# Performance work log

Measured on AMD Instinct MI355X. Metric: run time of the kernel, lower is better.

## Reference

```python
import jax, jax.numpy as jnp
import numpy as np

CUTOFF = 5.0           # module init kwarg
NSYS, NAT = 64, 1000   # 64 systems of 1000 atoms each
BOX = 21.544           # cubic box edge -> ~0.1 atoms/A^3 (water-like density)
MAX_PAIRS = 2_200_000


def setup_inputs() -> dict:
    key = jax.random.key(0)
    coords = jax.random.uniform(key, (NSYS * NAT, 3), dtype=jnp.float32) * BOX
    isys = jnp.repeat(jnp.arange(NSYS, dtype=jnp.int32), NAT)
    natoms = jnp.full((NSYS,), NAT, dtype=jnp.int32)
    return {"coordinates": coords, "isys": isys, "natoms": natoms}


def reference(coordinates, isys, natoms):
    # Fixed-capacity cutoff neighbor list (no PBC branch), faithful to
    # GraphGeneratorFixed: half-list (i<j, same system), squared distances d12,
    # compacted into a MAX_PAIRS buffer padded with padding_value=N, then
    # symmetrized by concatenation.
    nsys = natoms.shape[0]
    n = coordinates.shape[0]
    nat = n // nsys                      # equal-sized systems (static)
    padding_value = n
    cutoff2 = jnp.float32(CUTOFF * CUTOFF)

    x = coordinates.reshape(nsys, nat, 3)                 # [S, nat, 3]
    sq = jnp.sum(x * x, axis=-1)                          # [S, nat]
    gram = jnp.einsum('sid,sjd->sij', x, x)               # [S, nat, nat]
    d12 = sq[:, :, None] + sq[:, None, :] - 2.0 * gram    # squared distances

    triu = jnp.triu(jnp.ones((nat, nat), dtype=bool), k=1)  # i < j half-list
    mask = (d12 < cutoff2) & triu[None, :, :]             # [S, nat, nat]
    mflat = mask.reshape(-1)                              # [S*nat*nat]
    npairs = jnp.sum(mflat)

    # stream-compaction: position of each kept pair in the output buffer
    pos = jnp.cumsum(mflat.astype(jnp.int32)) - 1
    sel = jnp.where(mflat, pos, MAX_PAIRS)                # OOB -> dropped
    flat_idx = jnp.arange(nsys * nat * nat, dtype=jnp.int32)
    idx_buf = jnp.full((MAX_PAIRS,), -1, dtype=jnp.int32).at[sel].set(
        flat_idx, mode='drop')

    valid = idx_buf >= 0
    ib = jnp.maximum(idx_buf, 0)
    s = ib // (nat * nat)
    rem = ib % (nat * nat)
    i = rem // nat
    j = rem % nat
    src = jnp.where(valid, s * nat + i, padding_value)
    dst = jnp.where(valid, s * nat + j, padding_value)
    d12_sel = jnp.where(valid, d12.reshape(-1)[ib], cutoff2)

    # symmetrize (directed graph), as in the original
    edge_src = jnp.concatenate([src, dst])
    edge_dst = jnp.concatenate([dst, src])
    d12_out = jnp.concatenate([d12_sel, d12_sel])
    return edge_src, edge_dst, d12_out, npairs
```

## Files before the change

kernel.cpp:

```cpp
#include <hip/hip_runtime.h>

#define NSYS 64
#define NAT  1000
#define NTOT (NSYS * NAT)
#define MP   2200000
#define CUT2 25.0f
#define PADV 64000.0f
#define SCAN_BLOCKS 250
#define RPB  16
#define TILES ((NAT + RPB - 1) / RPB)
#define CAP  104

__device__ __forceinline__ float dist2f(float xi, float yi, float zi,
                                        float xj, float yj, float zj) {
    float dx = xi - xj, dy = yi - yj, dz = zi - zj;
    return fmaf(dz, dz, fmaf(dy, dy, dx * dx));
}

__global__ __launch_bounds__(1024) void k_eval(const float* __restrict__ coords,
                                               int* __restrict__ counts,
                                               uint2* __restrict__ qbuf) {
    __shared__ float lc[NAT * 3];
    int s    = blockIdx.x / TILES;
    int tile = blockIdx.x % TILES;
    const float* cs = coords + s * (NAT * 3);
    for (int idx = threadIdx.x; idx < NAT * 3; idx += 1024) lc[idx] = cs[idx];
    __syncthreads();
    int w    = threadIdx.x >> 6;
    int lane = threadIdx.x & 63;
    int r    = tile * RPB + w;
    if (r >= NAT) return;
    float xi = lc[3 * r], yi = lc[3 * r + 1], zi = lc[3 * r + 2];
    int grow = s * NAT + r;
    uint2* q = qbuf + (size_t)grow * CAP;
    int running = 0;
    unsigned long long lt = (1ull << lane) - 1ull;
    for (int j = r + 1 + lane; j < NAT; j += 64) {
        float d2 = dist2f(xi, yi, zi, lc[3 * j], lc[3 * j + 1], lc[3 * j + 2]);
        bool keep = d2 < CUT2;
        unsigned long long m = __ballot(keep);
        if (keep) {
            int rank = running + (int)__popcll(m & lt);
            if (rank < CAP)
                q[rank] = make_uint2((unsigned)(j - r), __float_as_uint(d2));
        }
        running += (int)__popcll(m);
    }
    if (lane == 0) counts[grow] = running;
}

__global__ void k_scan_a(const int* __restrict__ counts, int* __restrict__ offs,
                         int* __restrict__ bsum) {
    __shared__ int tmp[256];
    int t = threadIdx.x;
    int g = blockIdx.x * 256 + t;
    int v = counts[g];
    tmp[t] = v;
    __syncthreads();
    for (int off = 1; off < 256; off <<= 1) {
        int u = (t >= off) ? tmp[t - off] : 0;
        __syncthreads();
        tmp[t] += u;
        __syncthreads();
    }
    offs[g] = tmp[t] - v;
    if (t == 255) bsum[blockIdx.x] = tmp[255];
}

__global__ void k_scan_b(int* __restrict__ bsum, int* __restrict__ total) {
    __shared__ int tmp[256];
    int t = threadIdx.x;
    int v = (t < SCAN_BLOCKS) ? bsum[t] : 0;
    tmp[t] = v;
    __syncthreads();
    for (int off = 1; off < 256; off <<= 1) {
        int u = (t >= off) ? tmp[t - off] : 0;
        __syncthreads();
        tmp[t] += u;
        __syncthreads();
    }
    if (t < SCAN_BLOCKS) bsum[t] = tmp[t] - v;
    if (t == 255) *total = tmp[255];
}

__global__ void k_emit(const int* __restrict__ counts, const int* __restrict__ offs,
                       const int* __restrict__ bsum, const uint2* __restrict__ qbuf,
                       float* __restrict__ out) {
    int gt   = blockIdx.x * blockDim.x + threadIdx.x;
    int row  = gt >> 6;
    int lane = gt & 63;
    if (row >= NTOT) return;
    int off = offs[row] + bsum[row >> 8];
    int cnt = counts[row];
    if (cnt > CAP) cnt = CAP;
    const uint2* q = qbuf + (size_t)row * CAP;
    float fs = (float)row;
    for (int l = lane; l < cnt; l += 64) {
        uint2 e = q[l];
        int pos = off + l;
        if (pos < MP) {
            float fd = (float)(row + (int)e.x);
            float d2 = __uint_as_float(e.y);
            out[pos]          = fs;
            out[MP + pos]     = fd;
            out[2 * MP + pos] = fd;
            out[3 * MP + pos] = fs;
            out[4 * MP + pos] = d2;
            out[5 * MP + pos] = d2;
        }
    }
}

__global__ void k_pad(const int* __restrict__ total_p, float* __restrict__ out) {
    int k4 = (blockIdx.x * 256 + threadIdx.x) * 4;
    if (k4 >= MP) return;
    int total = *total_p;
    if (k4 == 0) out[6 * MP] = (float)total;
    int valid = total < MP ? total : MP;
    if (k4 + 4 <= valid) return;
    if (k4 >= valid) {
        float4 vp = {PADV, PADV, PADV, PADV};
        float4 vc = {CUT2, CUT2, CUT2, CUT2};
        *(float4*)(out + k4)          = vp;
        *(float4*)(out + MP + k4)     = vp;
        *(float4*)(out + 2 * MP + k4) = vp;
        *(float4*)(out + 3 * MP + k4) = vp;
        *(float4*)(out + 4 * MP + k4) = vc;
        *(float4*)(out + 5 * MP + k4) = vc;
    } else {
#pragma unroll
        for (int e = 0; e < 4; e++) {
            int k = k4 + e;
            if (k >= valid && k < MP) {
                out[k]          = PADV;
                out[MP + k]     = PADV;
                out[2 * MP + k] = PADV;
                out[3 * MP + k] = PADV;
                out[4 * MP + k] = CUT2;
                out[5 * MP + k] = CUT2;
            }
        }
    }
}

extern "C" void kernel_launch(void* const* d_in, const int* in_sizes, int n_in,
                              void* d_out, int out_size, void* d_ws, size_t ws_size,
                              hipStream_t stream) {
    const float* coords = (const float*)d_in[0];
    float* out = (float*)d_out;

    int*   counts = (int*)d_ws;
    int*   offs   = counts + NTOT;
    int*   bsum   = offs + NTOT;
    int*   total  = bsum + 256;
    uint2* qbuf   = (uint2*)(total + 16);

    k_eval<<<NSYS * TILES, 1024, 0, stream>>>(coords, counts, qbuf);
    k_scan_a<<<SCAN_BLOCKS, 256, 0, stream>>>(counts, offs, bsum);
    k_scan_b<<<1, 256, 0, stream>>>(bsum, total);
    k_emit<<<(NTOT * 64) / 256, 256, 0, stream>>>(counts, offs, bsum, qbuf, out);
    k_pad<<<(MP / 4 + 255) / 256, 256, 0, stream>>>(total, out);
}
```

Before: 121.0 us.

## Fuse block scan, emit and pad into persistent kernel; rebalance eval rows

The pair-evaluation kernel now uses eight persistent blocks per system. Rows are interleaved across warps so triangular workloads balance, coordinates are packed as float4 in shared memory, and each lane handles two candidates per iteration. The second-level scan, emit and pad kernels are merged into one persistent kernel that recomputes the block-prefix in shared memory. This cuts launch count and tail imbalance, at the cost of redundant small scans per block and less parallelism in emit.

```diff
diff --git a/kernel.cpp b/kernel.cpp
--- a/kernel.cpp
+++ b/kernel.cpp
@@ -7,9 +7,9 @@
 #define CUT2 25.0f
 #define PADV 64000.0f
 #define SCAN_BLOCKS 250
-#define RPB  16
-#define TILES ((NAT + RPB - 1) / RPB)
 #define CAP  104
+#define EB   512
+#define LCN  1152
 
 __device__ __forceinline__ float dist2f(float xi, float yi, float zi,
                                         float xj, float yj, float zj) {
@@ -20,33 +20,48 @@
 __global__ __launch_bounds__(1024) void k_eval(const float* __restrict__ coords,
                                                int* __restrict__ counts,
                                                uint2* __restrict__ qbuf) {
-    __shared__ float lc[NAT * 3];
-    int s    = blockIdx.x / TILES;
-    int tile = blockIdx.x % TILES;
+    __shared__ float4 lc[LCN];
+    int s      = blockIdx.x >> 3;
+    int stripe = blockIdx.x & 7;
     const float* cs = coords + s * (NAT * 3);
-    for (int idx = threadIdx.x; idx < NAT * 3; idx += 1024) lc[idx] = cs[idx];
+    for (int a = threadIdx.x; a < NAT; a += 1024)
+        lc[a] = make_float4(cs[3 * a], cs[3 * a + 1], cs[3 * a + 2], 0.0f);
     __syncthreads();
     int w    = threadIdx.x >> 6;
     int lane = threadIdx.x & 63;
-    int r    = tile * RPB + w;
-    if (r >= NAT) return;
-    float xi = lc[3 * r], yi = lc[3 * r + 1], zi = lc[3 * r + 2];
-    int grow = s * NAT + r;
-    uint2* q = qbuf + (size_t)grow * CAP;
-    int running = 0;
+    int W    = stripe * 16 + w;
     unsigned long long lt = (1ull << lane) - 1ull;
-    for (int j = r + 1 + lane; j < NAT; j += 64) {
-        float d2 = dist2f(xi, yi, zi, lc[3 * j], lc[3 * j + 1], lc[3 * j + 2]);
-        bool keep = d2 < CUT2;
-        unsigned long long m = __ballot(keep);
-        if (keep) {
-            int rank = running + (int)__popcll(m & lt);
-            if (rank < CAP)
-                q[rank] = make_uint2((unsigned)(j - r), __float_as_uint(d2));
+    for (int r = W; r < NAT; r += 128) {
+        float4 ci = lc[r];
+        int grow = s * NAT + r;
+        uint2* q = qbuf + (size_t)grow * CAP;
+        int running = 0;
+        for (int jb = r + 1; jb < NAT; jb += 128) {
+            int j  = jb + lane;
+            int j2 = j + 64;
+            float4 c0 = lc[j];
+            float4 c1 = lc[j2];
+            float d0 = dist2f(ci.x, ci.y, ci.z, c0.x, c0.y, c0.z);
+            float d1 = dist2f(ci.x, ci.y, ci.z, c1.x, c1.y, c1.z);
+            bool k0 = (j  < NAT) && (d0 < CUT2);
+            bool k1 = (j2 < NAT) && (d1 < CUT2);
+            unsigned long long m0 = __ballot(k0);
+            unsigned long long m1 = __ballot(k1);
+            if (k0) {
+                int rank = running + (int)__popcll(m0 & lt);
+                if (rank < CAP)
+                    q[rank] = make_uint2((unsigned)(j - r), __float_as_uint(d0));
+            }
+            int base1 = running + (int)__popcll(m0);
+            if (k1) {
+                int rank = base1 + (int)__popcll(m1 & lt);
+                if (rank < CAP)
+                    q[rank] = make_uint2((unsigned)(j2 - r), __float_as_uint(d1));
+            }
+            running = base1 + (int)__popcll(m1);
         }
-        running += (int)__popcll(m);
+        if (lane == 0) counts[grow] = running;
     }
-    if (lane == 0) counts[grow] = running;
 }
 
 __global__ void k_scan_a(const int* __restrict__ counts, int* __restrict__ offs,
@@ -67,77 +82,86 @@
     if (t == 255) bsum[blockIdx.x] = tmp[255];
 }
 
-__global__ void k_scan_b(int* __restrict__ bsum, int* __restrict__ total) {
-    __shared__ int tmp[256];
+__global__ __launch_bounds__(1024) void k_emitpad(const int* __restrict__ counts,
+                                                  const int* __restrict__ offs,
+                                                  const int* __restrict__ bsum,
+                                                  const uint2* __restrict__ qbuf,
+                                                  float* __restrict__ out) {
+    __shared__ int bpre[256];
+    __shared__ int stot;
     int t = threadIdx.x;
-    int v = (t < SCAN_BLOCKS) ? bsum[t] : 0;
-    tmp[t] = v;
+    int v = 0;
+    if (t < 256) {
+        v = (t < SCAN_BLOCKS) ? bsum[t] : 0;
+        bpre[t] = v;
+    }
     __syncthreads();
     for (int off = 1; off < 256; off <<= 1) {
-        int u = (t >= off) ? tmp[t - off] : 0;
+        int u = 0;
+        if (t < 256 && t >= off) u = bpre[t - off];
         __syncthreads();
-        tmp[t] += u;
+        if (t < 256) bpre[t] += u;
         __syncthreads();
     }
-    if (t < SCAN_BLOCKS) bsum[t] = tmp[t] - v;
-    if (t == 255) *total = tmp[255];
-}
+    int incl = (t < 256) ? bpre[t] : 0;
+    __syncthreads();
+    if (t < 256) bpre[t] = incl - v;
+    if (t == 255) stot = incl;
+    __syncthreads();
 
-__global__ void k_emit(const int* __restrict__ counts, const int* __restrict__ offs,
-                       const int* __restrict__ bsum, const uint2* __restrict__ qbuf,
-                       float* __restrict__ out) {
-    int gt   = blockIdx.x * blockDim.x + threadIdx.x;
-    int row  = gt >> 6;
-    int lane = gt & 63;
-    if (row >= NTOT) return;
-    int off = offs[row] + bsum[row >> 8];
-    int cnt = counts[row];
-    if (cnt > CAP) cnt = CAP;
-    const uint2* q = qbuf + (size_t)row * CAP;
-    float fs = (float)row;
-    for (int l = lane; l < cnt; l += 64) {
-        uint2 e = q[l];
-        int pos = off + l;
-        if (pos < MP) {
-            float fd = (float)(row + (int)e.x);
-            float d2 = __uint_as_float(e.y);
-            out[pos]          = fs;
-            out[MP + pos]     = fd;
-            out[2 * MP + pos] = fd;
-            out[3 * MP + pos] = fs;
-            out[4 * MP + pos] = d2;
-            out[5 * MP + pos] = d2;
+    int wv   = t >> 6;
+    int lane = t & 63;
+    int GW   = blockIdx.x * 16 + wv;
+    for (int r = GW; r < NTOT; r += EB * 16) {
+        int off = offs[r] + bpre[r >> 8];
+        int cnt = counts[r];
+        if (cnt > CAP) cnt = CAP;
+        const uint2* q = qbuf + (size_t)r * CAP;
+        float fs = (float)r;
+        for (int l = lane; l < cnt; l += 64) {
+            uint2 e = q[l];
+            int pos = off + l;
+            if (pos < MP) {
+                float fd = (float)(r + (int)e.x);
+                float d2 = __uint_as_float(e.y);
+                out[pos]          = fs;
+                out[MP + pos]     = fd;
+                out[2 * MP + pos] = fd;
+                out[3 * MP + pos] = fs;
+                out[4 * MP + pos] = d2;
+                out[5 * MP + pos] = d2;
+            }
         }
     }
-}
 
-__global__ void k_pad(const int* __restrict__ total_p, float* __restrict__ out) {
-    int k4 = (blockIdx.x * 256 + threadIdx.x) * 4;
-    if (k4 >= MP) return;
-    int total = *total_p;
-    if (k4 == 0) out[6 * MP] = (float)total;
+    int total = stot;
+    if (blockIdx.x == 0 && t == 0) out[6 * MP] = (float)total;
     int valid = total < MP ? total : MP;
-    if (k4 + 4 <= valid) return;
-    if (k4 >= valid) {
-        float4 vp = {PADV, PADV, PADV, PADV};
-        float4 vc = {CUT2, CUT2, CUT2, CUT2};
-        *(float4*)(out + k4)          = vp;
-        *(float4*)(out + MP + k4)     = vp;
-        *(float4*)(out + 2 * MP + k4) = vp;
-        *(float4*)(out + 3 * MP + k4) = vp;
-        *(float4*)(out + 4 * MP + k4) = vc;
-        *(float4*)(out + 5 * MP + k4) = vc;
-    } else {
+    const int NQ = MP / 4;
+    for (int q4 = blockIdx.x * 1024 + t; q4 < NQ; q4 += EB * 1024) {
+        int k4 = q4 * 4;
+        if (k4 + 4 <= valid) continue;
+        if (k4 >= valid) {
+            float4 vp = {PADV, PADV, PADV, PADV};
+            float4 vc = {CUT2, CUT2, CUT2, CUT2};
+            *(float4*)(out + k4)          = vp;
+            *(float4*)(out + MP + k4)     = vp;
+            *(float4*)(out + 2 * MP + k4) = vp;
+            *(float4*)(out + 3 * MP + k4) = vp;
+            *(float4*)(out + 4 * MP + k4) = vc;
+            *(float4*)(out + 5 * MP + k4) = vc;
+        } else {
 #pragma unroll
-        for (int e = 0; e < 4; e++) {
-            int k = k4 + e;
-            if (k >= valid && k < MP) {
-                out[k]          = PADV;
-                out[MP + k]     = PADV;
-                out[2 * MP + k] = PADV;
-                out[3 * MP + k] = PADV;
-                out[4 * MP + k] = CUT2;
-                out[5 * MP + k] = CUT2;
+            for (int e = 0; e < 4; e++) {
+                int k = k4 + e;
+                if (k >= valid && k < MP) {
+                    out[k]          = PADV;
+                    out[MP + k]     = PADV;
+                    out[2 * MP + k] = PADV;
+                    out[3 * MP + k] = PADV;
+                    out[4 * MP + k] = CUT2;
+                    out[5 * MP + k] = CUT2;
+                }
             }
         }
     }
@@ -152,12 +176,9 @@
     int*   counts = (int*)d_ws;
     int*   offs   = counts + NTOT;
     int*   bsum   = offs + NTOT;
-    int*   total  = bsum + 256;
-    uint2* qbuf   = (uint2*)(total + 16);
+    uint2* qbuf   = (uint2*)(bsum + 256);
 
-    k_eval<<<NSYS * TILES, 1024, 0, stream>>>(coords, counts, qbuf);
+    k_eval<<<EB, 1024, 0, stream>>>(coords, counts, qbuf);
     k_scan_a<<<SCAN_BLOCKS, 256, 0, stream>>>(counts, offs, bsum);
-    k_scan_b<<<1, 256, 0, stream>>>(bsum, total);
-    k_emit<<<(NTOT * 64) / 256, 256, 0, stream>>>(counts, offs, bsum, qbuf, out);
-    k_pad<<<(MP / 4 + 255) / 256, 256, 0, stream>>>(total, out);
+    k_emitpad<<<EB, 1024, 0, stream>>>(counts, offs, bsum, qbuf, out);
 }
```

After: 113.4 us. 6.3% less time.
